# Kernel tuning notes

Measured on AMD Instinct MI355X. Metric: run time of the kernel, lower is better.

Reference implementation:

```python
import jax, jax.numpy as jnp
import numpy as np

B, D, NF, L, G = 8192, 4096, 16, 32, 64  # batch, input_dim, num_factors, latent_per_factor, num groups
K = D // G  # group size (contiguous equal-size partition of columns)


def setup_inputs() -> dict:
    key = jax.random.key(0)
    k0, k1, k2, k3 = jax.random.split(key, 4)
    x = jax.random.normal(k0, (B, D), dtype=jnp.float32)
    # encoder: Linear(D,128) -> ReLU -> Linear(128, NF*L)
    W1 = jax.random.normal(k1, (D, 128), dtype=jnp.float32) * 0.02
    b1 = jnp.zeros((128,), dtype=jnp.float32)
    W2 = jax.random.normal(k2, (128, NF * L), dtype=jnp.float32) * 0.02
    b2 = jnp.zeros((NF * L,), dtype=jnp.float32)
    # k_matrix decoders: one [K, L] matrix per group, stacked -> [G, K, L]
    decoders = jax.random.normal(k3, (G, K, L), dtype=jnp.float32)
    return {"x": x, "W1": W1, "b1": b1, "W2": W2, "b2": b2, "decoders": decoders}


def reference(x, W1, b1, W2, b2, decoders):
    # encoder
    z = jax.nn.relu(x @ W1 + b1) @ W2 + b2                 # [B, NF*L]
    # reconstructions[:, group_g] = sum_j z_j @ D_g^T  ==  (sum_j z_j) @ D_g^T
    z_sum = z.reshape(x.shape[0], NF, L).sum(axis=1)        # [B, L]
    recon = jnp.einsum('bl,gkl->bgk', z_sum, decoders)      # [B, G, K]
    recon = recon.reshape(x.shape[0], G * K)                # [B, D] (contiguous groups)
    return (z, recon)
```

## Files before the change

kernel.cpp:

```cpp
#include <hip/hip_runtime.h>
#include <hip/hip_bf16.h>

#define BATCH 8192
#define DIN   4096
#define H1    128
#define NLAT  512
#define LAT   32
#define BM    16
#define PP    130

typedef short bf16x8 __attribute__((ext_vector_type(8)));
typedef short bf16x4 __attribute__((ext_vector_type(4)));
typedef float f32x4  __attribute__((ext_vector_type(4)));
typedef float f32x16 __attribute__((ext_vector_type(16)));

static __device__ __forceinline__ unsigned short f2bf(float f) {
  union { float f; unsigned u; } v; v.f = f;
  return (unsigned short)((v.u + 0x7FFFu + ((v.u >> 16) & 1u)) >> 16);
}
static __device__ __forceinline__ float bf2f(unsigned short u) {
  union { unsigned u; float f; } v; v.u = ((unsigned)u) << 16; return v.f;
}

__global__ void prep_all(const float* __restrict__ W1, const float* __restrict__ W2,
                         const float* __restrict__ dec,
                         unsigned short* __restrict__ W1B,
                         unsigned short* __restrict__ W2B,
                         unsigned short* __restrict__ decB) {
  int b = blockIdx.x;
  int t = threadIdx.x;
  int lane = t & 63;
  if (b < 256) {
    int g = lane >> 4, fr = lane & 15;
    int gi = (b << 2) + (t >> 6);
    int kb = ((gi >> 3) << 5) + (g << 3);
    int c = ((gi & 7) << 4) + fr;
    union { bf16x8 v; unsigned short u[8]; } o;
#pragma unroll
    for (int j = 0; j < 8; j++) o.u[j] = f2bf(W1[(size_t)(kb + j) * H1 + c]);
    *(bf16x8*)(W1B + (((size_t)gi << 6) + lane) * 8) = o.v;
  } else if (b < 288) {
    int g = lane >> 4, fr = lane & 15;
    int gi = ((b - 256) << 2) + (t >> 6);
    int kb = ((gi >> 5) << 5) + (g << 3);
    int c = ((gi & 31) << 4) + fr;
    union { bf16x8 v; unsigned short u[8]; } o;
#pragma unroll
    for (int j = 0; j < 8; j++) o.u[j] = f2bf(W2[(size_t)(kb + j) * NLAT + c]);
    *(bf16x8*)(W2B + (((size_t)gi << 6) + lane) * 8) = o.v;
  } else {
    int grp = ((b - 288) << 2) + (t >> 6);
    int cf = grp >> 1, q = grp & 1;
    int m = lane & 31, h = lane >> 5;
    const float* src = dec + ((size_t)(cf * 32 + m)) * LAT + q * 16 + h * 8;
    union { bf16x8 v; unsigned short u[8]; } o;
#pragma unroll
    for (int j = 0; j < 8; j++) o.u[j] = f2bf(src[j]);
    *(bf16x8*)(decB + (((size_t)grp << 6) + lane) * 8) = o.v;
  }
}

__global__ __launch_bounds__(512, 2) void enc_kernel(
    const float* __restrict__ x, const unsigned short* __restrict__ W1B,
    const unsigned short* __restrict__ W2B,
    const float* __restrict__ b1, const float* __restrict__ b2,
    float* __restrict__ zout, unsigned short* __restrict__ zsumb) {
  __shared__ unsigned short pacc[8 * BM * PP];
  __shared__ unsigned short hs[16 * 128];
  __shared__ float zsp[8 * BM * 33];

  const int t = threadIdx.x;
  const int rbase = blockIdx.x << 4;
  const int w = t >> 6, lane = t & 63;
  const int g = lane >> 4, fr = lane & 15;

  f32x4 acc[8];
#pragma unroll
  for (int i = 0; i < 8; i++) acc[i] = (f32x4){0.f, 0.f, 0.f, 0.f};

  const float* arow = x + (size_t)(rbase + fr) * DIN + (w << 9) + (g << 3);
#pragma unroll 4
  for (int c = 0; c < 16; ++c) {
    f32x4 a0 = *(const f32x4*)(arow + (c << 5));
    f32x4 a1 = *(const f32x4*)(arow + (c << 5) + 4);
    union { bf16x8 v; unsigned short u[8]; } af;
#pragma unroll
    for (int j = 0; j < 4; j++) { af.u[j] = f2bf(a0[j]); af.u[4 + j] = f2bf(a1[j]); }
    const unsigned short* bp =
        W1B + (((size_t)((w << 4) + c) << 3) << 9) + (lane << 3);
#pragma unroll
    for (int cf = 0; cf < 8; ++cf) {
      bf16x8 bv = *(const bf16x8*)(bp + ((size_t)cf << 9));
      acc[cf] = __builtin_amdgcn_mfma_f32_16x16x32_bf16(af.v, bv, acc[cf], 0, 0, 0);
    }
  }

#pragma unroll
  for (int cf = 0; cf < 8; ++cf)
#pragma unroll
    for (int j = 0; j < 4; ++j)
      pacc[(w * BM + (g << 2) + j) * PP + (cf << 4) + fr] = f2bf(acc[cf][j]);
  __syncthreads();

  {
    const int r = t >> 5, c4 = (t & 31) << 2;
    float s0 = b1[c4], s1 = b1[c4 + 1], s2 = b1[c4 + 2], s3 = b1[c4 + 3];
#pragma unroll
    for (int wv = 0; wv < 8; ++wv) {
      union { bf16x4 v; unsigned short u[4]; } p;
      p.v = *(const bf16x4*)&pacc[(wv * BM + r) * PP + c4];
      s0 += bf2f(p.u[0]); s1 += bf2f(p.u[1]); s2 += bf2f(p.u[2]); s3 += bf2f(p.u[3]);
    }
    union { bf16x4 v; unsigned short u[4]; } o;
    o.u[0] = f2bf(fmaxf(s0, 0.f)); o.u[1] = f2bf(fmaxf(s1, 0.f));
    o.u[2] = f2bf(fmaxf(s2, 0.f)); o.u[3] = f2bf(fmaxf(s3, 0.f));
    const int gi = c4 >> 3;
    *(bf16x4*)(hs + (r << 7) + ((gi ^ (r & 15)) << 3) + (c4 & 7)) = o.v;
  }
  __syncthreads();

  f32x4 acc2[4];
#pragma unroll
  for (int i = 0; i < 4; i++) acc2[i] = (f32x4){0.f, 0.f, 0.f, 0.f};
#pragma unroll
  for (int k32 = 0; k32 < 4; ++k32) {
    bf16x8 a0 = *(const bf16x8*)(hs + (fr << 7) +
                  ((((k32 << 2) + g) ^ (fr & 15)) << 3));
#pragma unroll
    for (int cc = 0; cc < 4; ++cc) {
      bf16x8 bv = *(const bf16x8*)(W2B +
          (((size_t)((k32 << 5) + (w << 2) + cc)) << 9) + (lane << 3));
      acc2[cc] = __builtin_amdgcn_mfma_f32_16x16x32_bf16(a0, bv, acc2[cc], 0, 0, 0);
    }
  }
  {
    f32x4 zv[4];
#pragma unroll
    for (int cc = 0; cc < 4; ++cc) {
      const float b2v = b2[(w << 6) + (cc << 4) + fr];
#pragma unroll
      for (int j = 0; j < 4; j++) zv[cc][j] = acc2[cc][j] + b2v;
    }
    const int row0 = g << 2;
#pragma unroll
    for (int j = 0; j < 4; j++) {
#pragma unroll
      for (int cc = 0; cc < 4; ++cc)
        zout[(size_t)(rbase + row0 + j) * NLAT + (w << 6) + (cc << 4) + fr] = zv[cc][j];
      zsp[(w * BM + row0 + j) * 33 + fr]      = zv[0][j] + zv[2][j];
      zsp[(w * BM + row0 + j) * 33 + 16 + fr] = zv[1][j] + zv[3][j];
    }
  }
  __syncthreads();
  {
    const int r = t >> 5, l = t & 31;
    float s = 0.f;
#pragma unroll
    for (int wv = 0; wv < 8; ++wv) s += zsp[(wv * BM + r) * 33 + l];
    zsumb[(size_t)(rbase + r) * LAT + l] = f2bf(s);
  }
}

__global__ __launch_bounds__(256) void recon_kernel(
    const unsigned short* __restrict__ zsumb, const unsigned short* __restrict__ decB,
    float* __restrict__ rout) {
  const int t = threadIdx.x;
  const int w = t >> 6, lane = t & 63;
  const int m = lane & 31, h = lane >> 5;
  const int rbase = (blockIdx.x >> 2) << 5;
  const int cfbase = ((blockIdx.x & 3) << 5) + (w << 3);

  const unsigned short* arow = zsumb + ((size_t)(rbase + m) << 5) + (h << 3);
  bf16x8 a0 = *(const bf16x8*)(arow);
  bf16x8 a1 = *(const bf16x8*)(arow + 16);

#pragma unroll 2
  for (int f = 0; f < 8; ++f) {
    const int cf = cfbase + f;
    bf16x8 bv0 = *(const bf16x8*)(decB + ((size_t)cf << 10) + (lane << 3));
    bf16x8 bv1 = *(const bf16x8*)(decB + ((size_t)cf << 10) + 512 + (lane << 3));
    f32x16 c;
#pragma unroll
    for (int i = 0; i < 16; ++i) c[i] = 0.f;
    c = __builtin_amdgcn_mfma_f32_32x32x16_bf16(a0, bv0, c, 0, 0, 0);
    c = __builtin_amdgcn_mfma_f32_32x32x16_bf16(a1, bv1, c, 0, 0, 0);
    const int colbase = (cf << 5) + m;
#pragma unroll
    for (int r = 0; r < 16; ++r) {
      const int row = rbase + (r & 3) + ((r >> 2) << 3) + (h << 2);
      rout[(size_t)row * DIN + colbase] = c[r];
    }
  }
}

extern "C" void kernel_launch(void* const* d_in, const int* in_sizes, int n_in,
                              void* d_out, int out_size, void* d_ws, size_t ws_size,
                              hipStream_t stream) {
  const float* x   = (const float*)d_in[0];
  const float* W1  = (const float*)d_in[1];
  const float* b1  = (const float*)d_in[2];
  const float* W2  = (const float*)d_in[3];
  const float* b2  = (const float*)d_in[4];
  const float* dec = (const float*)d_in[5];
  float* zout = (float*)d_out;
  float* rout = zout + (size_t)BATCH * NLAT;

  char* ws = (char*)d_ws;
  unsigned short* W1B   = (unsigned short*)ws;
  unsigned short* W2B   = (unsigned short*)(ws + (1u << 20));
  unsigned short* decB  = (unsigned short*)(ws + (1u << 20) + (128u << 10));
  unsigned short* zsumb = (unsigned short*)(ws + (1u << 20) + (384u << 10));

  prep_all<<<dim3(352), 256, 0, stream>>>(W1, W2, dec, W1B, W2B, decB);
  enc_kernel<<<dim3(BATCH / BM), 512, 0, stream>>>(x, W1B, W2B, b1, b2, zout, zsumb);
  recon_kernel<<<dim3(1024), 256, 0, stream>>>(zsumb, decB, rout);
}
```

Before: 84.68 us.

## Double encoder row tile to 32 with 16 waves sharing W1 fragments

The encoder block now covers 32 batch rows with 1024 threads, and each wave loads every W1 bf16 fragment once and feeds it to two MFMAs, one per 16-row half. The K-split drops from 512 to 256 columns per wave. The partial reductions from waves 0-7 and 8-15 are merged in shared memory in two phases, and the second GEMM is remapped over 16 waves. The change also swaps the manual bf16 rounding for the HIP intrinsic. It aims to halve W1 traffic per row, in exchange for larger LDS use (about 73KB), an extra sync and read-modify-write pass, and more register pressure under launch_bounds(1024,4).

```diff
diff --git a/kernel.cpp b/kernel.cpp
--- a/kernel.cpp
+++ b/kernel.cpp
@@ -6,7 +6,7 @@
 #define H1    128
 #define NLAT  512
 #define LAT   32
-#define BM    16
+#define BM    32
 #define PP    130
 
 typedef short bf16x8 __attribute__((ext_vector_type(8)));
@@ -15,8 +15,8 @@
 typedef float f32x16 __attribute__((ext_vector_type(16)));
 
 static __device__ __forceinline__ unsigned short f2bf(float f) {
-  union { float f; unsigned u; } v; v.f = f;
-  return (unsigned short)((v.u + 0x7FFFu + ((v.u >> 16) & 1u)) >> 16);
+  __hip_bfloat16 h = __float2bfloat16(f);
+  return *reinterpret_cast<unsigned short*>(&h);
 }
 static __device__ __forceinline__ float bf2f(unsigned short u) {
   union { unsigned u; float f; } v; v.u = ((unsigned)u) << 16; return v.f;
@@ -60,46 +60,73 @@
   }
 }
 
-__global__ __launch_bounds__(512, 2) void enc_kernel(
+__global__ __launch_bounds__(1024, 4) void enc_kernel(
     const float* __restrict__ x, const unsigned short* __restrict__ W1B,
     const unsigned short* __restrict__ W2B,
     const float* __restrict__ b1, const float* __restrict__ b2,
     float* __restrict__ zout, unsigned short* __restrict__ zsumb) {
-  __shared__ unsigned short pacc[8 * BM * PP];
-  __shared__ unsigned short hs[16 * 128];
-  __shared__ float zsp[8 * BM * 33];
+  __shared__ __align__(16) unsigned char smem[74752];
+  unsigned short* pacc = (unsigned short*)smem;
+  unsigned short* hs   = (unsigned short*)(smem + 66560);
+  float* zsp           = (float*)smem;
 
   const int t = threadIdx.x;
-  const int rbase = blockIdx.x << 4;
+  const int rbase = blockIdx.x << 5;
   const int w = t >> 6, lane = t & 63;
   const int g = lane >> 4, fr = lane & 15;
 
-  f32x4 acc[8];
-#pragma unroll
-  for (int i = 0; i < 8; i++) acc[i] = (f32x4){0.f, 0.f, 0.f, 0.f};
-
-  const float* arow = x + (size_t)(rbase + fr) * DIN + (w << 9) + (g << 3);
-#pragma unroll 4
-  for (int c = 0; c < 16; ++c) {
-    f32x4 a0 = *(const f32x4*)(arow + (c << 5));
-    f32x4 a1 = *(const f32x4*)(arow + (c << 5) + 4);
-    union { bf16x8 v; unsigned short u[8]; } af;
-#pragma unroll
-    for (int j = 0; j < 4; j++) { af.u[j] = f2bf(a0[j]); af.u[4 + j] = f2bf(a1[j]); }
+  f32x4 acc0[8], acc1[8];
+#pragma unroll
+  for (int i = 0; i < 8; i++) {
+    acc0[i] = (f32x4){0.f, 0.f, 0.f, 0.f};
+    acc1[i] = (f32x4){0.f, 0.f, 0.f, 0.f};
+  }
+  const float* arow0 = x + (size_t)(rbase + fr) * DIN + (w << 8) + (g << 3);
+  const float* arow1 = arow0 + ((size_t)DIN << 4);
+#pragma unroll 2
+  for (int c = 0; c < 8; ++c) {
+    f32x4 a0 = *(const f32x4*)(arow0 + (c << 5));
+    f32x4 a1 = *(const f32x4*)(arow0 + (c << 5) + 4);
+    f32x4 a2 = *(const f32x4*)(arow1 + (c << 5));
+    f32x4 a3 = *(const f32x4*)(arow1 + (c << 5) + 4);
+    union { bf16x8 v; unsigned short u[8]; } af0, af1;
+#pragma unroll
+    for (int j = 0; j < 4; j++) {
+      af0.u[j] = f2bf(a0[j]); af0.u[4 + j] = f2bf(a1[j]);
+      af1.u[j] = f2bf(a2[j]); af1.u[4 + j] = f2bf(a3[j]);
+    }
     const unsigned short* bp =
-        W1B + (((size_t)((w << 4) + c) << 3) << 9) + (lane << 3);
+        W1B + (((size_t)((((w << 3) + c) << 3))) << 9) + (lane << 3);
 #pragma unroll
     for (int cf = 0; cf < 8; ++cf) {
       bf16x8 bv = *(const bf16x8*)(bp + ((size_t)cf << 9));
-      acc[cf] = __builtin_amdgcn_mfma_f32_16x16x32_bf16(af.v, bv, acc[cf], 0, 0, 0);
-    }
-  }
-
-#pragma unroll
-  for (int cf = 0; cf < 8; ++cf)
-#pragma unroll
-    for (int j = 0; j < 4; ++j)
-      pacc[(w * BM + (g << 2) + j) * PP + (cf << 4) + fr] = f2bf(acc[cf][j]);
+      acc0[cf] = __builtin_amdgcn_mfma_f32_16x16x32_bf16(af0.v, bv, acc0[cf], 0, 0, 0);
+      acc1[cf] = __builtin_amdgcn_mfma_f32_16x16x32_bf16(af1.v, bv, acc1[cf], 0, 0, 0);
+    }
+  }
+
+  const int ws = w & 7;
+  if (w < 8) {
+#pragma unroll
+    for (int cf = 0; cf < 8; ++cf)
+#pragma unroll
+      for (int j = 0; j < 4; ++j) {
+        pacc[(ws * BM + (g << 2) + j) * PP + (cf << 4) + fr] = f2bf(acc0[cf][j]);
+        pacc[(ws * BM + 16 + (g << 2) + j) * PP + (cf << 4) + fr] = f2bf(acc1[cf][j]);
+      }
+  }
+  __syncthreads();
+  if (w >= 8) {
+#pragma unroll
+    for (int cf = 0; cf < 8; ++cf)
+#pragma unroll
+      for (int j = 0; j < 4; ++j) {
+        unsigned short* p0 = &pacc[(ws * BM + (g << 2) + j) * PP + (cf << 4) + fr];
+        unsigned short* p1 = &pacc[(ws * BM + 16 + (g << 2) + j) * PP + (cf << 4) + fr];
+        *p0 = f2bf(bf2f(*p0) + acc0[cf][j]);
+        *p1 = f2bf(bf2f(*p1) + acc1[cf][j]);
+      }
+  }
   __syncthreads();
 
   {
@@ -119,17 +146,18 @@
   }
   __syncthreads();
 
+  const int wr = w & 1, wc = w >> 1;
   f32x4 acc2[4];
 #pragma unroll
   for (int i = 0; i < 4; i++) acc2[i] = (f32x4){0.f, 0.f, 0.f, 0.f};
 #pragma unroll
   for (int k32 = 0; k32 < 4; ++k32) {
-    bf16x8 a0 = *(const bf16x8*)(hs + (fr << 7) +
-                  ((((k32 << 2) + g) ^ (fr & 15)) << 3));
+    bf16x8 a0 = *(const bf16x8*)(hs + (((wr << 4) + fr) << 7) +
+                  ((((k32 << 2) + g) ^ fr) << 3));
 #pragma unroll
     for (int cc = 0; cc < 4; ++cc) {
       bf16x8 bv = *(const bf16x8*)(W2B +
-          (((size_t)((k32 << 5) + (w << 2) + cc)) << 9) + (lane << 3));
+          (((size_t)((k32 << 5) + (wc << 2) + cc)) << 9) + (lane << 3));
       acc2[cc] = __builtin_amdgcn_mfma_f32_16x16x32_bf16(a0, bv, acc2[cc], 0, 0, 0);
     }
   }
@@ -137,26 +165,29 @@
     f32x4 zv[4];
 #pragma unroll
     for (int cc = 0; cc < 4; ++cc) {
-      const float b2v = b2[(w << 6) + (cc << 4) + fr];
+      const float b2v = b2[(wc << 6) + (cc << 4) + fr];
 #pragma unroll
       for (int j = 0; j < 4; j++) zv[cc][j] = acc2[cc][j] + b2v;
     }
     const int row0 = g << 2;
 #pragma unroll
     for (int j = 0; j < 4; j++) {
+      const int grow = rbase + (wr << 4) + row0 + j;
 #pragma unroll
       for (int cc = 0; cc < 4; ++cc)
-        zout[(size_t)(rbase + row0 + j) * NLAT + (w << 6) + (cc << 4) + fr] = zv[cc][j];
-      zsp[(w * BM + row0 + j) * 33 + fr]      = zv[0][j] + zv[2][j];
-      zsp[(w * BM + row0 + j) * 33 + 16 + fr] = zv[1][j] + zv[3][j];
+        zout[(size_t)grow * NLAT + (wc << 6) + (cc << 4) + fr] = zv[cc][j];
+      zsp[(w * 16 + row0 + j) * 33 + fr]      = zv[0][j] + zv[2][j];
+      zsp[(w * 16 + row0 + j) * 33 + 16 + fr] = zv[1][j] + zv[3][j];
     }
   }
   __syncthreads();
   {
     const int r = t >> 5, l = t & 31;
+    const int rh = r >> 4;
     float s = 0.f;
 #pragma unroll
-    for (int wv = 0; wv < 8; ++wv) s += zsp[(wv * BM + r) * 33 + l];
+    for (int wcv = 0; wcv < 8; ++wcv)
+      s += zsp[((((wcv << 1) | rh) << 4) + (r & 15)) * 33 + l];
     zsumb[(size_t)(rbase + r) * LAT + l] = f2bf(s);
   }
 }
@@ -212,6 +243,6 @@
   unsigned short* zsumb = (unsigned short*)(ws + (1u << 20) + (384u << 10));
 
   prep_all<<<dim3(352), 256, 0, stream>>>(W1, W2, dec, W1B, W2B, decB);
-  enc_kernel<<<dim3(BATCH / BM), 512, 0, stream>>>(x, W1B, W2B, b1, b2, zout, zsumb);
+  enc_kernel<<<dim3(BATCH / BM), 1024, 0, stream>>>(x, W1B, W2B, b1, b2, zout, zsumb);
   recon_kernel<<<dim3(1024), 256, 0, stream>>>(zsumb, decB, rout);
 }
```

New measurement: 77.02 us (median of 2 runs). -9.0%, faster.
